# Kernel tuning notes

Measured on AMD Instinct MI355X. Metric: run time of the kernel, lower is better.

## Reference

```python
import jax, jax.numpy as jnp
import numpy as np

N_NODES = 100000


def _gcn_conv(x, W, b, src, dst, num_nodes):
    """PyG-style GCNConv: add self-loops, symmetric normalization, linear.
    x: [N, Fin], W: [Fin, Fout], b: [Fout], src/dst: [E] (already include self-loops).
    """
    h = x @ W  # [N, Fout] transform first (PyG order), keeps edge traffic at Fout width
    ones = jnp.ones(dst.shape[0], dtype=h.dtype)
    deg = jax.ops.segment_sum(ones, dst, num_segments=num_nodes)  # degree of A+I
    dinv = jnp.where(deg > 0, jax.lax.rsqrt(deg), 0.0)
    norm = dinv[src] * dinv[dst]  # [E]
    msg = h[src] * norm[:, None]  # [E, Fout] gather + scale
    out = jax.ops.segment_sum(msg, dst, num_segments=num_nodes)  # scatter-add
    return out + b


def setup_inputs() -> dict:
    key = jax.random.key(0)
    k1, k2, k3, k4, k5 = jax.random.split(key, 5)
    input_dim, hidden_dim, embedding_dim = 128, 64, 32
    x = jax.random.normal(k1, (N_NODES, input_dim), dtype=jnp.float32)
    edge_index = jax.random.randint(k2, (2, 1600000), 0, N_NODES, dtype=jnp.int32)
    # Glorot-like init for weights
    W1 = jax.random.normal(k3, (input_dim, hidden_dim), dtype=jnp.float32) / np.sqrt(input_dim)
    b1 = jnp.zeros((hidden_dim,), dtype=jnp.float32)
    W2 = jax.random.normal(k4, (hidden_dim, embedding_dim), dtype=jnp.float32) / np.sqrt(hidden_dim)
    b2 = jnp.zeros((embedding_dim,), dtype=jnp.float32)
    return {"x": x, "edge_index": edge_index, "W1": W1, "b1": b1, "W2": W2, "b2": b2}


def reference(x, edge_index, W1, b1, W2, b2):
    num_nodes = x.shape[0]
    loop = jnp.arange(num_nodes, dtype=edge_index.dtype)
    src = jnp.concatenate([edge_index[0], loop])  # add self-loops (PyG default)
    dst = jnp.concatenate([edge_index[1], loop])
    h = _gcn_conv(x, W1, b1, src, dst, num_nodes)
    h = jax.nn.relu(h)
    z = _gcn_conv(h, W2, b2, src, dst, num_nodes)
    return z
```

## Files before the change

### kernel.cpp

```cpp
#include <hip/hip_runtime.h>
#include <hip/hip_bf16.h>


#define MAXBUCK 512

typedef unsigned int uint32;

__device__ __forceinline__ void fma4(float4& a, float s, const float4& w) {
    a.x = fmaf(s, w.x, a.x); a.y = fmaf(s, w.y, a.y);
    a.z = fmaf(s, w.z, a.z); a.w = fmaf(s, w.w, a.w);
}
__device__ __forceinline__ uint32 bf16rn(float f) {
    uint32 u = __float_as_uint(f);
    return (u + 0x7fffu + ((u >> 16) & 1u)) >> 16;
}
__device__ __forceinline__ float bflo(uint32 v) { return __uint_as_float(v << 16); }
__device__ __forceinline__ float bfhi(uint32 v) { return __uint_as_float(v & 0xffff0000u); }

__global__ void k_initcur(int* __restrict__ cursor, int nbuck, int cap) {
    int i = blockIdx.x * blockDim.x + threadIdx.x;
    if (i < nbuck) cursor[i] = i * cap;
}

__global__ __launch_bounds__(1024) void k_bin(const int* __restrict__ src,
                                              const int* __restrict__ dst, int E,
                                              int nbuck, int cap,
                                              int* __restrict__ cursor,
                                              uint32* __restrict__ pairs) {
    __shared__ int hist[MAXBUCK];
    __shared__ int base_l[MAXBUCK];
    __shared__ int cur[MAXBUCK];
    int t = threadIdx.x;
    int e0 = blockIdx.x * 4096;
    for (int i = t; i < MAXBUCK; i += 1024) { hist[i] = 0; cur[i] = 0; }
    __syncthreads();
    for (int i = t; i < 4096; i += 1024) {
        int e = e0 + i;
        if (e < E) atomicAdd(&hist[dst[e] >> 8], 1);
    }
    __syncthreads();
    for (int i = t; i < nbuck; i += 1024)
        base_l[i] = hist[i] ? atomicAdd(&cursor[i], hist[i]) : 0;
    __syncthreads();
    for (int i = t; i < 4096; i += 1024) {
        int e = e0 + i;
        if (e < E) {
            int d = dst[e];
            int b = d >> 8;
            int p = atomicAdd(&cur[b], 1);
            int idx = base_l[b] + p;
            if (idx < (b + 1) * cap)
                pairs[idx] = (uint32)src[e] | ((uint32)(d & 255) << 24);
        }
    }
}

__global__ __launch_bounds__(1024) void k_fill2(const uint32* __restrict__ pairs,
                                                const int* __restrict__ bucket_end,
                                                int cap, int N,
                                                int* __restrict__ srclist,
                                                int* __restrict__ rowstart,
                                                int* __restrict__ cnt,
                                                float* __restrict__ dinv) {
    __shared__ int hist[256];
    __shared__ int sh[256];
    __shared__ int rs_ex[256];
    __shared__ int cur[256];
    int b = blockIdx.x;
    int t = threadIdx.x;
    int start = b * cap;
    int end = min(bucket_end[b], start + cap);
    int node0 = b << 8;

    if (t < 256) { hist[t] = 0; cur[t] = 0; }
    __syncthreads();
    for (int e = start + t; e < end; e += 1024)
        atomicAdd(&hist[pairs[e] >> 24], 1);
    __syncthreads();
    int v = 0;
    if (t < 256) { v = hist[t]; sh[t] = v; }
    __syncthreads();
    for (int off = 1; off < 256; off <<= 1) {
        int tmp = 0;
        if (t < 256 && t >= off) tmp = sh[t - off];
        __syncthreads();
        if (t < 256) sh[t] += tmp;
        __syncthreads();
    }
    if (t < 256) {
        rs_ex[t] = sh[t] - v;
        int node = node0 + t;
        if (node < N) {
            rowstart[node] = start + rs_ex[t];
            cnt[node] = v;
            dinv[node] = rsqrtf((float)(v + 1));
        }
    }
    __syncthreads();
    for (int e = start + t; e < end; e += 1024) {
        uint32 pr = pairs[e];
        int dl = pr >> 24;
        int p = atomicAdd(&cur[dl], 1);
        srclist[start + rs_ex[dl] + p] = (int)(pr & 0x00FFFFFFu);
    }
}

__global__ __launch_bounds__(256) void k_gemm1(const float* __restrict__ x,
                                               const float* __restrict__ W1,
                                               const float* __restrict__ dinv,
                                               uint32* __restrict__ h1b, int n) {
    __shared__ float W1s[128 * 64];
    __shared__ float xs[32][132];
    int t = threadIdx.x;
    const float4* W1v = (const float4*)W1;
    float4* W1sv = (float4*)W1s;
    for (int i = t; i < 2048; i += 256) W1sv[i] = W1v[i];
    int node0 = blockIdx.x * 32;
    const float4* xv = (const float4*)x;
    for (int i = t; i < 1024; i += 256) {
        int nl = i >> 5, kq = i & 31;
        int node = node0 + nl;
        float4 v = make_float4(0.f, 0.f, 0.f, 0.f);
        if (node < n) v = xv[(size_t)node * 32 + kq];
        *(float4*)&xs[nl][kq * 4] = v;
    }
    __syncthreads();

    int tx = t & 15;
    int ty = t >> 4;
    int na = ty * 2, nb = na + 1;
    float4 acc0 = make_float4(0.f, 0.f, 0.f, 0.f);
    float4 acc1 = make_float4(0.f, 0.f, 0.f, 0.f);
    const float4* W1sq = (const float4*)W1s;
#pragma unroll 4
    for (int kq = 0; kq < 32; kq++) {
        float4 xa = *(const float4*)&xs[na][kq * 4];
        float4 xb = *(const float4*)&xs[nb][kq * 4];
        float4 w0 = W1sq[(kq * 4 + 0) * 16 + tx];
        float4 w1 = W1sq[(kq * 4 + 1) * 16 + tx];
        float4 w2 = W1sq[(kq * 4 + 2) * 16 + tx];
        float4 w3 = W1sq[(kq * 4 + 3) * 16 + tx];
        fma4(acc0, xa.x, w0); fma4(acc0, xa.y, w1);
        fma4(acc0, xa.z, w2); fma4(acc0, xa.w, w3);
        fma4(acc1, xb.x, w0); fma4(acc1, xb.y, w1);
        fma4(acc1, xb.z, w2); fma4(acc1, xb.w, w3);
    }
    int nA = node0 + na, nB = node0 + nb;
    if (nA < n) {
        float di = dinv[nA];
        uint2 pk = make_uint2(bf16rn(acc0.x * di) | (bf16rn(acc0.y * di) << 16),
                              bf16rn(acc0.z * di) | (bf16rn(acc0.w * di) << 16));
        ((uint2*)h1b)[(size_t)nA * 16 + tx] = pk;
    }
    if (nB < n) {
        float di = dinv[nB];
        uint2 pk = make_uint2(bf16rn(acc1.x * di) | (bf16rn(acc1.y * di) << 16),
                              bf16rn(acc1.z * di) | (bf16rn(acc1.w * di) << 16));
        ((uint2*)h1b)[(size_t)nB * 16 + tx] = pk;
    }
}

__global__ __launch_bounds__(256) void k_gather_l1(const int* __restrict__ rowstart,
                                                   const int* __restrict__ cnt,
                                                   const int* __restrict__ srclist,
                                                   const uint32* __restrict__ h1b,
                                                   const float* __restrict__ dinv,
                                                   const float* __restrict__ b1,
                                                   const float* __restrict__ W2,
                                                   unsigned short* __restrict__ h2b, int n) {
    __shared__ __align__(16) float W2s[64 * 32];
    __shared__ __align__(16) float hb[4][64];
    int t = threadIdx.x;
    {
        const float4* W2v = (const float4*)W2;
        float4* W2sv = (float4*)W2s;
        W2sv[t] = W2v[t];
        W2sv[t + 256] = W2v[t + 256];
    }
    int wid = t >> 6, lane = t & 63;
    int node = blockIdx.x * 4 + wid;
    bool valid = (node < n);
    int j = lane & 15, q = lane >> 4;

    int row = valid ? rowstart[node] : 0;
    int m_all = valid ? cnt[node] : 0;
    float di = valid ? dinv[node] : 0.0f;
    const uint2* h1v = (const uint2*)h1b;
    float a0 = 0.f, a1 = 0.f, a2 = 0.f, a3 = 0.f;
    for (int j0 = 0; j0 < m_all; j0 += 64) {
        int m = min(64, m_all - j0);
        int sidx = (lane < m) ? srclist[row + j0 + lane] : 0;
        int jj = 0;
        for (; jj + 16 <= m; jj += 16) {
            int s0 = __shfl(sidx, jj + q);
            int s1 = __shfl(sidx, jj + 4 + q);
            int s2 = __shfl(sidx, jj + 8 + q);
            int s3 = __shfl(sidx, jj + 12 + q);
            uint2 v0 = h1v[(size_t)s0 * 16 + j];
            uint2 v1 = h1v[(size_t)s1 * 16 + j];
            uint2 v2 = h1v[(size_t)s2 * 16 + j];
            uint2 v3 = h1v[(size_t)s3 * 16 + j];
            a0 += (bflo(v0.x) + bflo(v1.x)) + (bflo(v2.x) + bflo(v3.x));
            a1 += (bfhi(v0.x) + bfhi(v1.x)) + (bfhi(v2.x) + bfhi(v3.x));
            a2 += (bflo(v0.y) + bflo(v1.y)) + (bflo(v2.y) + bflo(v3.y));
            a3 += (bfhi(v0.y) + bfhi(v1.y)) + (bfhi(v2.y) + bfhi(v3.y));
        }
        for (; jj + 8 <= m; jj += 8) {
            int s0 = __shfl(sidx, jj + q);
            int s1 = __shfl(sidx, jj + 4 + q);
            uint2 v0 = h1v[(size_t)s0 * 16 + j];
            uint2 v1 = h1v[(size_t)s1 * 16 + j];
            a0 += bflo(v0.x) + bflo(v1.x);
            a1 += bfhi(v0.x) + bfhi(v1.x);
            a2 += bflo(v0.y) + bflo(v1.y);
            a3 += bfhi(v0.y) + bfhi(v1.y);
        }
        for (; jj < m; jj += 4) {
            int jidx = jj + q;
            int s = __shfl(sidx, min(jidx, m - 1));
            uint2 v = h1v[(size_t)s * 16 + j];
            if (jidx < m) {
                a0 += bflo(v.x); a1 += bfhi(v.x);
                a2 += bflo(v.y); a3 += bfhi(v.y);
            }
        }
    }
    a0 += __shfl_xor(a0, 16); a0 += __shfl_xor(a0, 32);
    a1 += __shfl_xor(a1, 16); a1 += __shfl_xor(a1, 32);
    a2 += __shfl_xor(a2, 16); a2 += __shfl_xor(a2, 32);
    a3 += __shfl_xor(a3, 16); a3 += __shfl_xor(a3, 32);
    if (valid && q == 0) {
        uint2 sv = h1v[(size_t)node * 16 + j];
        float4 bq = ((const float4*)b1)[j];
        float4 hv;
        hv.x = fmaxf((a0 + bflo(sv.x)) * di + bq.x, 0.0f);
        hv.y = fmaxf((a1 + bfhi(sv.x)) * di + bq.y, 0.0f);
        hv.z = fmaxf((a2 + bflo(sv.y)) * di + bq.z, 0.0f);
        hv.w = fmaxf((a3 + bfhi(sv.y)) * di + bq.w, 0.0f);
        *(float4*)&hb[wid][4 * j] = hv;
    }
    __syncthreads();
    if (valid) {
        int c = lane & 31, half = lane >> 5;
        int k0 = half * 32;
        float s = 0.0f;
        const float4* hb4 = (const float4*)&hb[wid][k0];
#pragma unroll
        for (int kk = 0; kk < 8; kk++) {
            float4 h4 = hb4[kk];
            int kb = k0 + kk * 4;
            s = fmaf(h4.x, W2s[(kb + 0) * 32 + c], s);
            s = fmaf(h4.y, W2s[(kb + 1) * 32 + c], s);
            s = fmaf(h4.z, W2s[(kb + 2) * 32 + c], s);
            s = fmaf(h4.w, W2s[(kb + 3) * 32 + c], s);
        }
        s += __shfl_xor(s, 32);
        if (half == 0) h2b[(size_t)node * 32 + c] = (unsigned short)bf16rn(s * di);
    }
}

__global__ __launch_bounds__(256) void k_gather_l2(const int* __restrict__ rowstart,
                                                   const int* __restrict__ cnt,
                                                   const int* __restrict__ srclist,
                                                   const uint32* __restrict__ h2b,
                                                   const float* __restrict__ dinv,
                                                   const float* __restrict__ b2v,
                                                   float* __restrict__ out, int n) {
    int t = threadIdx.x;
    int wid = t >> 6, lane = t & 63;
    int node = blockIdx.x * 4 + wid;
    if (node >= n) return;
    int j = lane & 7, o = lane >> 3;

    int row = rowstart[node], m_all = cnt[node];
    float di = dinv[node];
    const uint2* h2v = (const uint2*)h2b;
    float a0 = 0.f, a1 = 0.f, a2 = 0.f, a3 = 0.f;
    for (int j0 = 0; j0 < m_all; j0 += 64) {
        int m = min(64, m_all - j0);
        int sidx = (lane < m) ? srclist[row + j0 + lane] : 0;
        int jj = 0;
        for (; jj + 16 <= m; jj += 16) {
            int s0 = __shfl(sidx, jj + o);
            int s1 = __shfl(sidx, jj + 8 + o);
            uint2 v0 = h2v[(size_t)s0 * 8 + j];
            uint2 v1 = h2v[(size_t)s1 * 8 + j];
            a0 += bflo(v0.x) + bflo(v1.x);
            a1 += bfhi(v0.x) + bfhi(v1.x);
            a2 += bflo(v0.y) + bflo(v1.y);
            a3 += bfhi(v0.y) + bfhi(v1.y);
        }
        for (; jj + 8 <= m; jj += 8) {
            int s0 = __shfl(sidx, jj + o);
            uint2 v0 = h2v[(size_t)s0 * 8 + j];
            a0 += bflo(v0.x); a1 += bfhi(v0.x);
            a2 += bflo(v0.y); a3 += bfhi(v0.y);
        }
        if (jj < m) {
            int jidx = jj + o;
            int s = __shfl(sidx, min(jidx, m - 1));
            uint2 v = h2v[(size_t)s * 8 + j];
            if (jidx < m) {
                a0 += bflo(v.x); a1 += bfhi(v.x);
                a2 += bflo(v.y); a3 += bfhi(v.y);
            }
        }
    }
    a0 += __shfl_xor(a0, 8); a0 += __shfl_xor(a0, 16); a0 += __shfl_xor(a0, 32);
    a1 += __shfl_xor(a1, 8); a1 += __shfl_xor(a1, 16); a1 += __shfl_xor(a1, 32);
    a2 += __shfl_xor(a2, 8); a2 += __shfl_xor(a2, 16); a2 += __shfl_xor(a2, 32);
    a3 += __shfl_xor(a3, 8); a3 += __shfl_xor(a3, 16); a3 += __shfl_xor(a3, 32);
    if (o == 0) {
        float di2 = di;
        uint2 sv = h2v[(size_t)node * 8 + j];
        float4 bq = ((const float4*)b2v)[j];
        float4 ov;
        ov.x = (a0 + bflo(sv.x)) * di2 + bq.x;
        ov.y = (a1 + bfhi(sv.x)) * di2 + bq.y;
        ov.z = (a2 + bflo(sv.y)) * di2 + bq.z;
        ov.w = (a3 + bfhi(sv.y)) * di2 + bq.w;
        ((float4*)out)[(size_t)node * 8 + j] = ov;
    }
}

extern "C" void kernel_launch(void* const* d_in, const int* in_sizes, int n_in,
                              void* d_out, int out_size, void* d_ws, size_t ws_size,
                              hipStream_t stream) {
    const float* x  = (const float*)d_in[0];
    const int*   ei = (const int*)d_in[1];
    const float* W1 = (const float*)d_in[2];
    const float* b1 = (const float*)d_in[3];
    const float* W2 = (const float*)d_in[4];
    const float* b2 = (const float*)d_in[5];
    float* out = (float*)d_out;

    const int N = in_sizes[0] / 128;
    const int E = in_sizes[1] / 2;
    const int* src = ei;
    const int* dst = ei + E;
    const int nbuck = (N + 255) >> 8;

    int mean = (E + nbuck - 1) / nbuck;
    int cap = (mean + (mean >> 3) + 256 + 63) & ~63;
    size_t region = (size_t)nbuck * cap;

    char* p = (char*)d_ws;
    uint32* pairs      = (uint32*)p;    p += region * 4;
    int* srclist       = (int*)p;       p += region * 4;
    uint32* h1b        = (uint32*)p;    p += (size_t)N * 64 * 2;
    uint32* h2b        = (uint32*)p;    p += (size_t)N * 32 * 2;
    int* cursor        = (int*)p;       p += MAXBUCK * 4;
    int* rowstart      = (int*)p;       p += (size_t)N * 4;
    int* cnt           = (int*)p;       p += (size_t)N * 4;
    float* dinv        = (float*)p;     p += (size_t)N * 4;

    k_initcur<<<(nbuck + 255) / 256, 256, 0, stream>>>(cursor, nbuck, cap);
    k_bin<<<(E + 4095) / 4096, 1024, 0, stream>>>(src, dst, E, nbuck, cap, cursor, pairs);
    k_fill2<<<nbuck, 1024, 0, stream>>>(pairs, cursor, cap, N, srclist, rowstart, cnt, dinv);

    k_gemm1<<<(N + 31) / 32, 256, 0, stream>>>(x, W1, dinv, h1b, N);
    k_gather_l1<<<(N + 3) / 4, 256, 0, stream>>>(rowstart, cnt, srclist, h1b, dinv,
                                                 b1, W2, (unsigned short*)h2b, N);
    k_gather_l2<<<(N + 3) / 4, 256, 0, stream>>>(rowstart, cnt, srclist, h2b, dinv,
                                                 b2, out, N);
}
```

Measured before the change: 252.0 us.

## Gather four nodes per wavefront, pack node metadata, pad bucket cursors, split GEMM staging

```diff
diff --git a/kernel.cpp b/kernel.cpp
--- a/kernel.cpp
+++ b/kernel.cpp
@@ -3,6 +3,7 @@
 
 
 #define MAXBUCK 512
+#define CURSTRIDE 16
 
 typedef unsigned int uint32;
 
@@ -16,11 +17,6 @@
 }
 __device__ __forceinline__ float bflo(uint32 v) { return __uint_as_float(v << 16); }
 __device__ __forceinline__ float bfhi(uint32 v) { return __uint_as_float(v & 0xffff0000u); }
-
-__global__ void k_initcur(int* __restrict__ cursor, int nbuck, int cap) {
-    int i = blockIdx.x * blockDim.x + threadIdx.x;
-    if (i < nbuck) cursor[i] = i * cap;
-}
 
 __global__ __launch_bounds__(1024) void k_bin(const int* __restrict__ src,
                                               const int* __restrict__ dst, int E,
@@ -30,22 +26,27 @@
     __shared__ int hist[MAXBUCK];
     __shared__ int base_l[MAXBUCK];
     __shared__ int cur[MAXBUCK];
+    __shared__ int dloc[4096];
     int t = threadIdx.x;
     int e0 = blockIdx.x * 4096;
     for (int i = t; i < MAXBUCK; i += 1024) { hist[i] = 0; cur[i] = 0; }
-    __syncthreads();
-    for (int i = t; i < 4096; i += 1024) {
-        int e = e0 + i;
-        if (e < E) atomicAdd(&hist[dst[e] >> 8], 1);
-    }
-    __syncthreads();
-    for (int i = t; i < nbuck; i += 1024)
-        base_l[i] = hist[i] ? atomicAdd(&cursor[i], hist[i]) : 0;
     __syncthreads();
     for (int i = t; i < 4096; i += 1024) {
         int e = e0 + i;
         if (e < E) {
             int d = dst[e];
+            dloc[i] = d;
+            atomicAdd(&hist[d >> 8], 1);
+        }
+    }
+    __syncthreads();
+    for (int i = t; i < nbuck; i += 1024)
+        base_l[i] = hist[i] ? (i * cap + atomicAdd(&cursor[i * CURSTRIDE], hist[i])) : 0;
+    __syncthreads();
+    for (int i = t; i < 4096; i += 1024) {
+        int e = e0 + i;
+        if (e < E) {
+            int d = dloc[i];
             int b = d >> 8;
             int p = atomicAdd(&cur[b], 1);
             int idx = base_l[b] + p;
@@ -56,11 +57,10 @@
 }
 
 __global__ __launch_bounds__(1024) void k_fill2(const uint32* __restrict__ pairs,
-                                                const int* __restrict__ bucket_end,
+                                                const int* __restrict__ bucket_cnt,
                                                 int cap, int N,
                                                 int* __restrict__ srclist,
-                                                int* __restrict__ rowstart,
-                                                int* __restrict__ cnt,
+                                                int4* __restrict__ meta,
                                                 float* __restrict__ dinv) {
     __shared__ int hist[256];
     __shared__ int sh[256];
@@ -69,7 +69,7 @@
     int b = blockIdx.x;
     int t = threadIdx.x;
     int start = b * cap;
-    int end = min(bucket_end[b], start + cap);
+    int end = start + min(bucket_cnt[b * CURSTRIDE], cap);
     int node0 = b << 8;
 
     if (t < 256) { hist[t] = 0; cur[t] = 0; }
@@ -91,9 +91,9 @@
         rs_ex[t] = sh[t] - v;
         int node = node0 + t;
         if (node < N) {
-            rowstart[node] = start + rs_ex[t];
-            cnt[node] = v;
-            dinv[node] = rsqrtf((float)(v + 1));
+            float dv = rsqrtf((float)(v + 1));
+            meta[node] = make_int4(start + rs_ex[t], v, __float_as_int(dv), 0);
+            dinv[node] = dv;
         }
     }
     __syncthreads();
@@ -109,41 +109,45 @@
                                                const float* __restrict__ W1,
                                                const float* __restrict__ dinv,
                                                uint32* __restrict__ h1b, int n) {
-    __shared__ float W1s[128 * 64];
-    __shared__ float xs[32][132];
+    __shared__ float W1s[64 * 64];
+    __shared__ float xs[32][68];
     int t = threadIdx.x;
-    const float4* W1v = (const float4*)W1;
-    float4* W1sv = (float4*)W1s;
-    for (int i = t; i < 2048; i += 256) W1sv[i] = W1v[i];
     int node0 = blockIdx.x * 32;
-    const float4* xv = (const float4*)x;
-    for (int i = t; i < 1024; i += 256) {
-        int nl = i >> 5, kq = i & 31;
-        int node = node0 + nl;
-        float4 v = make_float4(0.f, 0.f, 0.f, 0.f);
-        if (node < n) v = xv[(size_t)node * 32 + kq];
-        *(float4*)&xs[nl][kq * 4] = v;
-    }
-    __syncthreads();
-
     int tx = t & 15;
     int ty = t >> 4;
     int na = ty * 2, nb = na + 1;
     float4 acc0 = make_float4(0.f, 0.f, 0.f, 0.f);
     float4 acc1 = make_float4(0.f, 0.f, 0.f, 0.f);
+    const float4* W1v = (const float4*)W1;
+    const float4* xv = (const float4*)x;
+    float4* W1sv = (float4*)W1s;
     const float4* W1sq = (const float4*)W1s;
+
+#pragma unroll 1
+    for (int ph = 0; ph < 2; ph++) {
+        __syncthreads();
+        for (int i = t; i < 1024; i += 256) W1sv[i] = W1v[ph * 1024 + i];
+        for (int i = t; i < 512; i += 256) {
+            int nl = i >> 4, kq4 = i & 15;
+            int node = node0 + nl;
+            float4 v = make_float4(0.f, 0.f, 0.f, 0.f);
+            if (node < n) v = xv[(size_t)node * 32 + ph * 16 + kq4];
+            *(float4*)&xs[nl][kq4 * 4] = v;
+        }
+        __syncthreads();
 #pragma unroll 4
-    for (int kq = 0; kq < 32; kq++) {
-        float4 xa = *(const float4*)&xs[na][kq * 4];
-        float4 xb = *(const float4*)&xs[nb][kq * 4];
-        float4 w0 = W1sq[(kq * 4 + 0) * 16 + tx];
-        float4 w1 = W1sq[(kq * 4 + 1) * 16 + tx];
-        float4 w2 = W1sq[(kq * 4 + 2) * 16 + tx];
-        float4 w3 = W1sq[(kq * 4 + 3) * 16 + tx];
-        fma4(acc0, xa.x, w0); fma4(acc0, xa.y, w1);
-        fma4(acc0, xa.z, w2); fma4(acc0, xa.w, w3);
-        fma4(acc1, xb.x, w0); fma4(acc1, xb.y, w1);
-        fma4(acc1, xb.z, w2); fma4(acc1, xb.w, w3);
+        for (int kq = 0; kq < 16; kq++) {
+            float4 xa = *(const float4*)&xs[na][kq * 4];
+            float4 xb = *(const float4*)&xs[nb][kq * 4];
+            float4 w0 = W1sq[(kq * 4 + 0) * 16 + tx];
+            float4 w1 = W1sq[(kq * 4 + 1) * 16 + tx];
+            float4 w2 = W1sq[(kq * 4 + 2) * 16 + tx];
+            float4 w3 = W1sq[(kq * 4 + 3) * 16 + tx];
+            fma4(acc0, xa.x, w0); fma4(acc0, xa.y, w1);
+            fma4(acc0, xa.z, w2); fma4(acc0, xa.w, w3);
+            fma4(acc1, xb.x, w0); fma4(acc1, xb.y, w1);
+            fma4(acc1, xb.z, w2); fma4(acc1, xb.w, w3);
+        }
     }
     int nA = node0 + na, nB = node0 + nb;
     if (nA < n) {
@@ -160,16 +164,62 @@
     }
 }
 
-__global__ __launch_bounds__(256) void k_gather_l1(const int* __restrict__ rowstart,
-                                                   const int* __restrict__ cnt,
+__device__ __forceinline__ void drain_l1(int sidx, int jj, int m0,
+                                         const uint2* __restrict__ h1v, int j, int q,
+                                         float& a0, float& a1, float& a2, float& a3) {
+    for (; jj + 8 <= m0; jj += 8) {
+        int s0 = __shfl(sidx, jj + q), s1 = __shfl(sidx, jj + 4 + q);
+        uint2 v0 = h1v[(size_t)s0 * 16 + j], v1 = h1v[(size_t)s1 * 16 + j];
+        a0 += bflo(v0.x) + bflo(v1.x);
+        a1 += bfhi(v0.x) + bfhi(v1.x);
+        a2 += bflo(v0.y) + bflo(v1.y);
+        a3 += bfhi(v0.y) + bfhi(v1.y);
+    }
+    for (; jj < m0; jj += 4) {
+        int jidx = jj + q;
+        int s = __shfl(sidx, min(jidx, m0 - 1));
+        uint2 v = h1v[(size_t)s * 16 + j];
+        if (jidx < m0) {
+            a0 += bflo(v.x); a1 += bfhi(v.x);
+            a2 += bflo(v.y); a3 += bfhi(v.y);
+        }
+    }
+}
+__device__ __forceinline__ void extra_l1(const int* __restrict__ srclist, int row, int m_all,
+                                         int lane, const uint2* __restrict__ h1v, int j, int q,
+                                         float& a0, float& a1, float& a2, float& a3) {
+    for (int j0 = 64; j0 < m_all; j0 += 64) {
+        int m = min(64, m_all - j0);
+        int sb = (lane < m) ? srclist[row + j0 + lane] : 0;
+        int jj = 0;
+        for (; jj + 8 <= m; jj += 8) {
+            int s0 = __shfl(sb, jj + q), s1 = __shfl(sb, jj + 4 + q);
+            uint2 v0 = h1v[(size_t)s0 * 16 + j], v1 = h1v[(size_t)s1 * 16 + j];
+            a0 += bflo(v0.x) + bflo(v1.x);
+            a1 += bfhi(v0.x) + bfhi(v1.x);
+            a2 += bflo(v0.y) + bflo(v1.y);
+            a3 += bfhi(v0.y) + bfhi(v1.y);
+        }
+        for (; jj < m; jj += 4) {
+            int jidx = jj + q;
+            int s = __shfl(sb, min(jidx, m - 1));
+            uint2 v = h1v[(size_t)s * 16 + j];
+            if (jidx < m) {
+                a0 += bflo(v.x); a1 += bfhi(v.x);
+                a2 += bflo(v.y); a3 += bfhi(v.y);
+            }
+        }
+    }
+}
+
+__global__ __launch_bounds__(256) void k_gather_l1(const int4* __restrict__ meta,
                                                    const int* __restrict__ srclist,
                                                    const uint32* __restrict__ h1b,
-                                                   const float* __restrict__ dinv,
                                                    const float* __restrict__ b1,
                                                    const float* __restrict__ W2,
                                                    unsigned short* __restrict__ h2b, int n) {
     __shared__ __align__(16) float W2s[64 * 32];
-    __shared__ __align__(16) float hb[4][64];
+    __shared__ __align__(16) float hb[16][64];
     int t = threadIdx.x;
     {
         const float4* W2v = (const float4*)W2;
@@ -178,73 +228,121 @@
         W2sv[t + 256] = W2v[t + 256];
     }
     int wid = t >> 6, lane = t & 63;
-    int node = blockIdx.x * 4 + wid;
-    bool valid = (node < n);
+    int nA = blockIdx.x * 16 + wid * 4;
+    int nB = nA + 1, nC = nA + 2, nD = nA + 3;
+    bool vA = (nA < n), vB = (nB < n), vC = (nC < n), vD = (nD < n);
     int j = lane & 15, q = lane >> 4;
-
-    int row = valid ? rowstart[node] : 0;
-    int m_all = valid ? cnt[node] : 0;
-    float di = valid ? dinv[node] : 0.0f;
+    float4 bq = ((const float4*)b1)[j];
+
+    int rowA = 0, mA = 0, rowB = 0, mB = 0, rowC = 0, mC = 0, rowD = 0, mD = 0;
+    float diA = 0.f, diB = 0.f, diC = 0.f, diD = 0.f;
+    uint2 svA = make_uint2(0u, 0u), svB = svA, svC = svA, svD = svA;
     const uint2* h1v = (const uint2*)h1b;
-    float a0 = 0.f, a1 = 0.f, a2 = 0.f, a3 = 0.f;
-    for (int j0 = 0; j0 < m_all; j0 += 64) {
-        int m = min(64, m_all - j0);
-        int sidx = (lane < m) ? srclist[row + j0 + lane] : 0;
-        int jj = 0;
-        for (; jj + 16 <= m; jj += 16) {
-            int s0 = __shfl(sidx, jj + q);
-            int s1 = __shfl(sidx, jj + 4 + q);
-            int s2 = __shfl(sidx, jj + 8 + q);
-            int s3 = __shfl(sidx, jj + 12 + q);
-            uint2 v0 = h1v[(size_t)s0 * 16 + j];
-            uint2 v1 = h1v[(size_t)s1 * 16 + j];
-            uint2 v2 = h1v[(size_t)s2 * 16 + j];
-            uint2 v3 = h1v[(size_t)s3 * 16 + j];
-            a0 += (bflo(v0.x) + bflo(v1.x)) + (bflo(v2.x) + bflo(v3.x));
-            a1 += (bfhi(v0.x) + bfhi(v1.x)) + (bfhi(v2.x) + bfhi(v3.x));
-            a2 += (bflo(v0.y) + bflo(v1.y)) + (bflo(v2.y) + bflo(v3.y));
-            a3 += (bfhi(v0.y) + bfhi(v1.y)) + (bfhi(v2.y) + bfhi(v3.y));
-        }
-        for (; jj + 8 <= m; jj += 8) {
-            int s0 = __shfl(sidx, jj + q);
-            int s1 = __shfl(sidx, jj + 4 + q);
-            uint2 v0 = h1v[(size_t)s0 * 16 + j];
-            uint2 v1 = h1v[(size_t)s1 * 16 + j];
-            a0 += bflo(v0.x) + bflo(v1.x);
-            a1 += bfhi(v0.x) + bfhi(v1.x);
-            a2 += bflo(v0.y) + bflo(v1.y);
-            a3 += bfhi(v0.y) + bfhi(v1.y);
-        }
-        for (; jj < m; jj += 4) {
-            int jidx = jj + q;
-            int s = __shfl(sidx, min(jidx, m - 1));
-            uint2 v = h1v[(size_t)s * 16 + j];
-            if (jidx < m) {
-                a0 += bflo(v.x); a1 += bfhi(v.x);
-                a2 += bflo(v.y); a3 += bfhi(v.y);
-            }
-        }
-    }
-    a0 += __shfl_xor(a0, 16); a0 += __shfl_xor(a0, 32);
-    a1 += __shfl_xor(a1, 16); a1 += __shfl_xor(a1, 32);
-    a2 += __shfl_xor(a2, 16); a2 += __shfl_xor(a2, 32);
-    a3 += __shfl_xor(a3, 16); a3 += __shfl_xor(a3, 32);
-    if (valid && q == 0) {
-        uint2 sv = h1v[(size_t)node * 16 + j];
-        float4 bq = ((const float4*)b1)[j];
+    if (vA) { int4 mv = meta[nA]; rowA = mv.x; mA = mv.y; diA = __int_as_float(mv.z);
+              svA = h1v[(size_t)nA * 16 + j]; }
+    if (vB) { int4 mv = meta[nB]; rowB = mv.x; mB = mv.y; diB = __int_as_float(mv.z);
+              svB = h1v[(size_t)nB * 16 + j]; }
+    if (vC) { int4 mv = meta[nC]; rowC = mv.x; mC = mv.y; diC = __int_as_float(mv.z);
+              svC = h1v[(size_t)nC * 16 + j]; }
+    if (vD) { int4 mv = meta[nD]; rowD = mv.x; mD = mv.y; diD = __int_as_float(mv.z);
+              svD = h1v[(size_t)nD * 16 + j]; }
+    int cA = min(64, mA), cB = min(64, mB), cC = min(64, mC), cD = min(64, mD);
+    int sxA = (lane < cA) ? srclist[rowA + lane] : 0;
+    int sxB = (lane < cB) ? srclist[rowB + lane] : 0;
+    int sxC = (lane < cC) ? srclist[rowC + lane] : 0;
+    int sxD = (lane < cD) ? srclist[rowD + lane] : 0;
+
+    float aA0 = 0.f, aA1 = 0.f, aA2 = 0.f, aA3 = 0.f;
+    float aB0 = 0.f, aB1 = 0.f, aB2 = 0.f, aB3 = 0.f;
+    float aC0 = 0.f, aC1 = 0.f, aC2 = 0.f, aC3 = 0.f;
+    float aD0 = 0.f, aD1 = 0.f, aD2 = 0.f, aD3 = 0.f;
+    int jA = 0, jB = 0, jC = 0, jD = 0;
+    for (; jA + 8 <= cA && jB + 8 <= cB && jC + 8 <= cC && jD + 8 <= cD;
+           jA += 8, jB += 8, jC += 8, jD += 8) {
+        int sA0 = __shfl(sxA, jA + q), sA1 = __shfl(sxA, jA + 4 + q);
+        int sB0 = __shfl(sxB, jB + q), sB1 = __shfl(sxB, jB + 4 + q);
+        int sC0 = __shfl(sxC, jC + q), sC1 = __shfl(sxC, jC + 4 + q);
+        int sD0 = __shfl(sxD, jD + q), sD1 = __shfl(sxD, jD + 4 + q);
+        uint2 vA0 = h1v[(size_t)sA0 * 16 + j], vA1 = h1v[(size_t)sA1 * 16 + j];
+        uint2 vB0 = h1v[(size_t)sB0 * 16 + j], vB1 = h1v[(size_t)sB1 * 16 + j];
+        uint2 vC0 = h1v[(size_t)sC0 * 16 + j], vC1 = h1v[(size_t)sC1 * 16 + j];
+        uint2 vD0 = h1v[(size_t)sD0 * 16 + j], vD1 = h1v[(size_t)sD1 * 16 + j];
+        aA0 += bflo(vA0.x) + bflo(vA1.x); aA1 += bfhi(vA0.x) + bfhi(vA1.x);
+        aA2 += bflo(vA0.y) + bflo(vA1.y); aA3 += bfhi(vA0.y) + bfhi(vA1.y);
+        aB0 += bflo(vB0.x) + bflo(vB1.x); aB1 += bfhi(vB0.x) + bfhi(vB1.x);
+        aB2 += bflo(vB0.y) + bflo(vB1.y); aB3 += bfhi(vB0.y) + bfhi(vB1.y);
+        aC0 += bflo(vC0.x) + bflo(vC1.x); aC1 += bfhi(vC0.x) + bfhi(vC1.x);
+        aC2 += bflo(vC0.y) + bflo(vC1.y); aC3 += bfhi(vC0.y) + bfhi(vC1.y);
+        aD0 += bflo(vD0.x) + bflo(vD1.x); aD1 += bfhi(vD0.x) + bfhi(vD1.x);
+        aD2 += bflo(vD0.y) + bflo(vD1.y); aD3 += bfhi(vD0.y) + bfhi(vD1.y);
+    }
+    drain_l1(sxA, jA, cA, h1v, j, q, aA0, aA1, aA2, aA3);
+    drain_l1(sxB, jB, cB, h1v, j, q, aB0, aB1, aB2, aB3);
+    drain_l1(sxC, jC, cC, h1v, j, q, aC0, aC1, aC2, aC3);
+    drain_l1(sxD, jD, cD, h1v, j, q, aD0, aD1, aD2, aD3);
+    extra_l1(srclist, rowA, mA, lane, h1v, j, q, aA0, aA1, aA2, aA3);
+    extra_l1(srclist, rowB, mB, lane, h1v, j, q, aB0, aB1, aB2, aB3);
+    extra_l1(srclist, rowC, mC, lane, h1v, j, q, aC0, aC1, aC2, aC3);
+    extra_l1(srclist, rowD, mD, lane, h1v, j, q, aD0, aD1, aD2, aD3);
+
+    aA0 += __shfl_xor(aA0, 16); aA0 += __shfl_xor(aA0, 32);
+    aA1 += __shfl_xor(aA1, 16); aA1 += __shfl_xor(aA1, 32);
+    aA2 += __shfl_xor(aA2, 16); aA2 += __shfl_xor(aA2, 32);
+    aA3 += __shfl_xor(aA3, 16); aA3 += __shfl_xor(aA3, 32);
+    aB0 += __shfl_xor(aB0, 16); aB0 += __shfl_xor(aB0, 32);
+    aB1 += __shfl_xor(aB1, 16); aB1 += __shfl_xor(aB1, 32);
+    aB2 += __shfl_xor(aB2, 16); aB2 += __shfl_xor(aB2, 32);
+    aB3 += __shfl_xor(aB3, 16); aB3 += __shfl_xor(aB3, 32);
+    aC0 += __shfl_xor(aC0, 16); aC0 += __shfl_xor(aC0, 32);
+    aC1 += __shfl_xor(aC1, 16); aC1 += __shfl_xor(aC1, 32);
+    aC2 += __shfl_xor(aC2, 16); aC2 += __shfl_xor(aC2, 32);
+    aC3 += __shfl_xor(aC3, 16); aC3 += __shfl_xor(aC3, 32);
+    aD0 += __shfl_xor(aD0, 16); aD0 += __shfl_xor(aD0, 32);
+    aD1 += __shfl_xor(aD1, 16); aD1 += __shfl_xor(aD1, 32);
+    aD2 += __shfl_xor(aD2, 16); aD2 += __shfl_xor(aD2, 32);
+    aD3 += __shfl_xor(aD3, 16); aD3 += __shfl_xor(aD3, 32);
+    if (vA && q == 0) {
         float4 hv;
-        hv.x = fmaxf((a0 + bflo(sv.x)) * di + bq.x, 0.0f);
-        hv.y = fmaxf((a1 + bfhi(sv.x)) * di + bq.y, 0.0f);
-        hv.z = fmaxf((a2 + bflo(sv.y)) * di + bq.z, 0.0f);
-        hv.w = fmaxf((a3 + bfhi(sv.y)) * di + bq.w, 0.0f);
-        *(float4*)&hb[wid][4 * j] = hv;
-    }
-    __syncthreads();
-    if (valid) {
-        int c = lane & 31, half = lane >> 5;
-        int k0 = half * 32;
+        hv.x = fmaxf((aA0 + bflo(svA.x)) * diA + bq.x, 0.0f);
+        hv.y = fmaxf((aA1 + bfhi(svA.x)) * diA + bq.y, 0.0f);
+        hv.z = fmaxf((aA2 + bflo(svA.y)) * diA + bq.z, 0.0f);
+        hv.w = fmaxf((aA3 + bfhi(svA.y)) * diA + bq.w, 0.0f);
+        *(float4*)&hb[wid * 4 + 0][4 * j] = hv;
+    }
+    if (vB && q == 0) {
+        float4 hv;
+        hv.x = fmaxf((aB0 + bflo(svB.x)) * diB + bq.x, 0.0f);
+        hv.y = fmaxf((aB1 + bfhi(svB.x)) * diB + bq.y, 0.0f);
+        hv.z = fmaxf((aB2 + bflo(svB.y)) * diB + bq.z, 0.0f);
+        hv.w = fmaxf((aB3 + bfhi(svB.y)) * diB + bq.w, 0.0f);
+        *(float4*)&hb[wid * 4 + 1][4 * j] = hv;
+    }
+    if (vC && q == 0) {
+        float4 hv;
+        hv.x = fmaxf((aC0 + bflo(svC.x)) * diC + bq.x, 0.0f);
+        hv.y = fmaxf((aC1 + bfhi(svC.x)) * diC + bq.y, 0.0f);
+        hv.z = fmaxf((aC2 + bflo(svC.y)) * diC + bq.z, 0.0f);
+        hv.w = fmaxf((aC3 + bfhi(svC.y)) * diC + bq.w, 0.0f);
+        *(float4*)&hb[wid * 4 + 2][4 * j] = hv;
+    }
+    if (vD && q == 0) {
+        float4 hv;
+        hv.x = fmaxf((aD0 + bflo(svD.x)) * diD + bq.x, 0.0f);
+        hv.y = fmaxf((aD1 + bfhi(svD.x)) * diD + bq.y, 0.0f);
+        hv.z = fmaxf((aD2 + bflo(svD.y)) * diD + bq.z, 0.0f);
+        hv.w = fmaxf((aD3 + bfhi(svD.y)) * diD + bq.w, 0.0f);
+        *(float4*)&hb[wid * 4 + 3][4 * j] = hv;
+    }
+    __syncthreads();
+    int c = lane & 31, half = lane >> 5;
+    int k0 = half * 32;
+#pragma unroll
+    for (int nd = 0; nd < 4; nd++) {
+        int node = nA + nd;
+        if (node >= n) break;
+        float di = (nd == 0) ? diA : (nd == 1) ? diB : (nd == 2) ? diC : diD;
         float s = 0.0f;
-        const float4* hb4 = (const float4*)&hb[wid][k0];
+        const float4* hb4 = (const float4*)&hb[wid * 4 + nd][k0];
 #pragma unroll
         for (int kk = 0; kk < 8; kk++) {
             float4 h4 = hb4[kk];
@@ -259,46 +357,41 @@
     }
 }
 
-__global__ __launch_bounds__(256) void k_gather_l2(const int* __restrict__ rowstart,
-                                                   const int* __restrict__ cnt,
-                                                   const int* __restrict__ srclist,
-                                                   const uint32* __restrict__ h2b,
-                                                   const float* __restrict__ dinv,
-                                                   const float* __restrict__ b2v,
-                                                   float* __restrict__ out, int n) {
-    int t = threadIdx.x;
-    int wid = t >> 6, lane = t & 63;
-    int node = blockIdx.x * 4 + wid;
-    if (node >= n) return;
-    int j = lane & 7, o = lane >> 3;
-
-    int row = rowstart[node], m_all = cnt[node];
-    float di = dinv[node];
-    const uint2* h2v = (const uint2*)h2b;
-    float a0 = 0.f, a1 = 0.f, a2 = 0.f, a3 = 0.f;
-    for (int j0 = 0; j0 < m_all; j0 += 64) {
+__device__ __forceinline__ void drain_l2(int sidx, int jj, int m0,
+                                         const uint2* __restrict__ h2v, int j, int o,
+                                         float& a0, float& a1, float& a2, float& a3) {
+    for (; jj + 8 <= m0; jj += 8) {
+        int s0 = __shfl(sidx, jj + o);
+        uint2 v0 = h2v[(size_t)s0 * 8 + j];
+        a0 += bflo(v0.x); a1 += bfhi(v0.x);
+        a2 += bflo(v0.y); a3 += bfhi(v0.y);
+    }
+    if (jj < m0) {
+        int jidx = jj + o;
+        int s = __shfl(sidx, min(jidx, m0 - 1));
+        uint2 v = h2v[(size_t)s * 8 + j];
+        if (jidx < m0) {
+            a0 += bflo(v.x); a1 += bfhi(v.x);
+            a2 += bflo(v.y); a3 += bfhi(v.y);
+        }
+    }
+}
+__device__ __forceinline__ void extra_l2(const int* __restrict__ srclist, int row, int m_all,
+                                         int lane, const uint2* __restrict__ h2v, int j, int o,
+                                         float& a0, float& a1, float& a2, float& a3) {
+    for (int j0 = 64; j0 < m_all; j0 += 64) {
         int m = min(64, m_all - j0);
-        int sidx = (lane < m) ? srclist[row + j0 + lane] : 0;
+        int sb = (lane < m) ? srclist[row + j0 + lane] : 0;
         int jj = 0;
-        for (; jj + 16 <= m; jj += 16) {
-            int s0 = __shfl(sidx, jj + o);
-            int s1 = __shfl(sidx, jj + 8 + o);
-            uint2 v0 = h2v[(size_t)s0 * 8 + j];
-            uint2 v1 = h2v[(size_t)s1 * 8 + j];
-            a0 += bflo(v0.x) + bflo(v1.x);
-            a1 += bfhi(v0.x) + bfhi(v1.x);
-            a2 += bflo(v0.y) + bflo(v1.y);
-            a3 += bfhi(v0.y) + bfhi(v1.y);
-        }
         for (; jj + 8 <= m; jj += 8) {
-            int s0 = __shfl(sidx, jj + o);
+            int s0 = __shfl(sb, jj + o);
             uint2 v0 = h2v[(size_t)s0 * 8 + j];
             a0 += bflo(v0.x); a1 += bfhi(v0.x);
             a2 += bflo(v0.y); a3 += bfhi(v0.y);
         }
         if (jj < m) {
             int jidx = jj + o;
-            int s = __shfl(sidx, min(jidx, m - 1));
+            int s = __shfl(sb, min(jidx, m - 1));
             uint2 v = h2v[(size_t)s * 8 + j];
             if (jidx < m) {
                 a0 += bflo(v.x); a1 += bfhi(v.x);
@@ -306,20 +399,122 @@
             }
         }
     }
-    a0 += __shfl_xor(a0, 8); a0 += __shfl_xor(a0, 16); a0 += __shfl_xor(a0, 32);
-    a1 += __shfl_xor(a1, 8); a1 += __shfl_xor(a1, 16); a1 += __shfl_xor(a1, 32);
-    a2 += __shfl_xor(a2, 8); a2 += __shfl_xor(a2, 16); a2 += __shfl_xor(a2, 32);
-    a3 += __shfl_xor(a3, 8); a3 += __shfl_xor(a3, 16); a3 += __shfl_xor(a3, 32);
+}
+
+__global__ __launch_bounds__(256) void k_gather_l2(const int4* __restrict__ meta,
+                                                   const int* __restrict__ srclist,
+                                                   const uint32* __restrict__ h2b,
+                                                   const float* __restrict__ b2v,
+                                                   float* __restrict__ out, int n) {
+    int t = threadIdx.x;
+    int wid = t >> 6, lane = t & 63;
+    int nA = blockIdx.x * 16 + wid * 4;
+    if (nA >= n) return;
+    int nB = nA + 1, nC = nA + 2, nD = nA + 3;
+    bool vB_ = (nB < n), vC_ = (nC < n), vD_ = (nD < n);
+    int j = lane & 7, o = lane >> 3;
+    float4 bq = ((const float4*)b2v)[j];
+
+    const uint2* h2v = (const uint2*)h2b;
+    int4 mvA = meta[nA];
+    int rowA = mvA.x, mA = mvA.y;
+    float diA = __int_as_float(mvA.z);
+    uint2 svA = h2v[(size_t)nA * 8 + j];
+    int rowB = 0, mB = 0, rowC = 0, mC = 0, rowD = 0, mD = 0;
+    float diB = 0.f, diC = 0.f, diD = 0.f;
+    uint2 svB = make_uint2(0u, 0u), svC = svB, svD = svB;
+    if (vB_) { int4 mv = meta[nB]; rowB = mv.x; mB = mv.y; diB = __int_as_float(mv.z);
+               svB = h2v[(size_t)nB * 8 + j]; }
+    if (vC_) { int4 mv = meta[nC]; rowC = mv.x; mC = mv.y; diC = __int_as_float(mv.z);
+               svC = h2v[(size_t)nC * 8 + j]; }
+    if (vD_) { int4 mv = meta[nD]; rowD = mv.x; mD = mv.y; diD = __int_as_float(mv.z);
+               svD = h2v[(size_t)nD * 8 + j]; }
+    int cA = min(64, mA), cB = min(64, mB), cC = min(64, mC), cD = min(64, mD);
+    int sxA = (lane < cA) ? srclist[rowA + lane] : 0;
+    int sxB = (lane < cB) ? srclist[rowB + lane] : 0;
+    int sxC = (lane < cC) ? srclist[rowC + lane] : 0;
+    int sxD = (lane < cD) ? srclist[rowD + lane] : 0;
+
+    float aA0 = 0.f, aA1 = 0.f, aA2 = 0.f, aA3 = 0.f;
+    float aB0 = 0.f, aB1 = 0.f, aB2 = 0.f, aB3 = 0.f;
+    float aC0 = 0.f, aC1 = 0.f, aC2 = 0.f, aC3 = 0.f;
+    float aD0 = 0.f, aD1 = 0.f, aD2 = 0.f, aD3 = 0.f;
+    int jA = 0, jB = 0, jC = 0, jD = 0;
+    for (; jA + 8 <= cA && jB + 8 <= cB && jC + 8 <= cC && jD + 8 <= cD;
+           jA += 8, jB += 8, jC += 8, jD += 8) {
+        int sA0 = __shfl(sxA, jA + o);
+        int sB0 = __shfl(sxB, jB + o);
+        int sC0 = __shfl(sxC, jC + o);
+        int sD0 = __shfl(sxD, jD + o);
+        uint2 vA0 = h2v[(size_t)sA0 * 8 + j];
+        uint2 vB0 = h2v[(size_t)sB0 * 8 + j];
+        uint2 vC0 = h2v[(size_t)sC0 * 8 + j];
+        uint2 vD0 = h2v[(size_t)sD0 * 8 + j];
+        aA0 += bflo(vA0.x); aA1 += bfhi(vA0.x);
+        aA2 += bflo(vA0.y); aA3 += bfhi(vA0.y);
+        aB0 += bflo(vB0.x); aB1 += bfhi(vB0.x);
+        aB2 += bflo(vB0.y); aB3 += bfhi(vB0.y);
+        aC0 += bflo(vC0.x); aC1 += bfhi(vC0.x);
+        aC2 += bflo(vC0.y); aC3 += bfhi(vC0.y);
+        aD0 += bflo(vD0.x); aD1 += bfhi(vD0.x);
+        aD2 += bflo(vD0.y); aD3 += bfhi(vD0.y);
+    }
+    drain_l2(sxA, jA, cA, h2v, j, o, aA0, aA1, aA2, aA3);
+    drain_l2(sxB, jB, cB, h2v, j, o, aB0, aB1, aB2, aB3);
+    drain_l2(sxC, jC, cC, h2v, j, o, aC0, aC1, aC2, aC3);
+    drain_l2(sxD, jD, cD, h2v, j, o, aD0, aD1, aD2, aD3);
+    extra_l2(srclist, rowA, mA, lane, h2v, j, o, aA0, aA1, aA2, aA3);
+    extra_l2(srclist, rowB, mB, lane, h2v, j, o, aB0, aB1, aB2, aB3);
+    extra_l2(srclist, rowC, mC, lane, h2v, j, o, aC0, aC1, aC2, aC3);
+    extra_l2(srclist, rowD, mD, lane, h2v, j, o, aD0, aD1, aD2, aD3);
+
+    aA0 += __shfl_xor(aA0, 8); aA0 += __shfl_xor(aA0, 16); aA0 += __shfl_xor(aA0, 32);
+    aA1 += __shfl_xor(aA1, 8); aA1 += __shfl_xor(aA1, 16); aA1 += __shfl_xor(aA1, 32);
+    aA2 += __shfl_xor(aA2, 8); aA2 += __shfl_xor(aA2, 16); aA2 += __shfl_xor(aA2, 32);
+    aA3 += __shfl_xor(aA3, 8); aA3 += __shfl_xor(aA3, 16); aA3 += __shfl_xor(aA3, 32);
+    aB0 += __shfl_xor(aB0, 8); aB0 += __shfl_xor(aB0, 16); aB0 += __shfl_xor(aB0, 32);
+    aB1 += __shfl_xor(aB1, 8); aB1 += __shfl_xor(aB1, 16); aB1 += __shfl_xor(aB1, 32);
+    aB2 += __shfl_xor(aB2, 8); aB2 += __shfl_xor(aB2, 16); aB2 += __shfl_xor(aB2, 32);
+    aB3 += __shfl_xor(aB3, 8); aB3 += __shfl_xor(aB3, 16); aB3 += __shfl_xor(aB3, 32);
+    aC0 += __shfl_xor(aC0, 8); aC0 += __shfl_xor(aC0, 16); aC0 += __shfl_xor(aC0, 32);
+    aC1 += __shfl_xor(aC1, 8); aC1 += __shfl_xor(aC1, 16); aC1 += __shfl_xor(aC1, 32);
+    aC2 += __shfl_xor(aC2, 8); aC2 += __shfl_xor(aC2, 16); aC2 += __shfl_xor(aC2, 32);
+    aC3 += __shfl_xor(aC3, 8); aC3 += __shfl_xor(aC3, 16); aC3 += __shfl_xor(aC3, 32);
+    aD0 += __shfl_xor(aD0, 8); aD0 += __shfl_xor(aD0, 16); aD0 += __shfl_xor(aD0, 32);
+    aD1 += __shfl_xor(aD1, 8); aD1 += __shfl_xor(aD1, 16); aD1 += __shfl_xor(aD1, 32);
+    aD2 += __shfl_xor(aD2, 8); aD2 += __shfl_xor(aD2, 16); aD2 += __shfl_xor(aD2, 32);
+    aD3 += __shfl_xor(aD3, 8); aD3 += __shfl_xor(aD3, 16); aD3 += __shfl_xor(aD3, 32);
     if (o == 0) {
-        float di2 = di;
-        uint2 sv = h2v[(size_t)node * 8 + j];
-        float4 bq = ((const float4*)b2v)[j];
         float4 ov;
-        ov.x = (a0 + bflo(sv.x)) * di2 + bq.x;
-        ov.y = (a1 + bfhi(sv.x)) * di2 + bq.y;
-        ov.z = (a2 + bflo(sv.y)) * di2 + bq.z;
-        ov.w = (a3 + bfhi(sv.y)) * di2 + bq.w;
-        ((float4*)out)[(size_t)node * 8 + j] = ov;
+        ov.x = (aA0 + bflo(svA.x)) * diA + bq.x;
+        ov.y = (aA1 + bfhi(svA.x)) * diA + bq.y;
+        ov.z = (aA2 + bflo(svA.y)) * diA + bq.z;
+        ov.w = (aA3 + bfhi(svA.y)) * diA + bq.w;
+        ((float4*)out)[(size_t)nA * 8 + j] = ov;
+        if (vB_) {
+            float4 ob;
+            ob.x = (aB0 + bflo(svB.x)) * diB + bq.x;
+            ob.y = (aB1 + bfhi(svB.x)) * diB + bq.y;
+            ob.z = (aB2 + bflo(svB.y)) * diB + bq.z;
+            ob.w = (aB3 + bfhi(svB.y)) * diB + bq.w;
+            ((float4*)out)[(size_t)nB * 8 + j] = ob;
+        }
+        if (vC_) {
+            float4 oc;
+            oc.x = (aC0 + bflo(svC.x)) * diC + bq.x;
+            oc.y = (aC1 + bfhi(svC.x)) * diC + bq.y;
+            oc.z = (aC2 + bflo(svC.y)) * diC + bq.z;
+            oc.w = (aC3 + bfhi(svC.y)) * diC + bq.w;
+            ((float4*)out)[(size_t)nC * 8 + j] = oc;
+        }
+        if (vD_) {
+            float4 od;
+            od.x = (aD0 + bflo(svD.x)) * diD + bq.x;
+            od.y = (aD1 + bfhi(svD.x)) * diD + bq.y;
+            od.z = (aD2 + bflo(svD.y)) * diD + bq.z;
+            od.w = (aD3 + bfhi(svD.y)) * diD + bq.w;
+            ((float4*)out)[(size_t)nD * 8 + j] = od;
+        }
     }
 }
 
@@ -349,18 +544,16 @@
     int* srclist       = (int*)p;       p += region * 4;
     uint32* h1b        = (uint32*)p;    p += (size_t)N * 64 * 2;
     uint32* h2b        = (uint32*)p;    p += (size_t)N * 32 * 2;
-    int* cursor        = (int*)p;       p += MAXBUCK * 4;
-    int* rowstart      = (int*)p;       p += (size_t)N * 4;
-    int* cnt           = (int*)p;       p += (size_t)N * 4;
+    int* cursor        = (int*)p;       p += MAXBUCK * CURSTRIDE * 4;
+    int4* meta         = (int4*)p;      p += (size_t)N * 16;
     float* dinv        = (float*)p;     p += (size_t)N * 4;
 
-    k_initcur<<<(nbuck + 255) / 256, 256, 0, stream>>>(cursor, nbuck, cap);
+    hipMemsetAsync(cursor, 0, (size_t)nbuck * CURSTRIDE * 4, stream);
     k_bin<<<(E + 4095) / 4096, 1024, 0, stream>>>(src, dst, E, nbuck, cap, cursor, pairs);
-    k_fill2<<<nbuck, 1024, 0, stream>>>(pairs, cursor, cap, N, srclist, rowstart, cnt, dinv);
+    k_fill2<<<nbuck, 1024, 0, stream>>>(pairs, cursor, cap, N, srclist, meta, dinv);
 
     k_gemm1<<<(N + 31) / 32, 256, 0, stream>>>(x, W1, dinv, h1b, N);
-    k_gather_l1<<<(N + 3) / 4, 256, 0, stream>>>(rowstart, cnt, srclist, h1b, dinv,
-                                                 b1, W2, (unsigned short*)h2b, N);
-    k_gather_l2<<<(N + 3) / 4, 256, 0, stream>>>(rowstart, cnt, srclist, h2b, dinv,
-                                                 b2, out, N);
-}
+    k_gather_l1<<<(N + 15) / 16, 256, 0, stream>>>(meta, srclist, h1b,
+                                                   b1, W2, (unsigned short*)h2b, N);
+    k_gather_l2<<<(N + 15) / 16, 256, 0, stream>>>(meta, srclist, h2b, b2, out, N);
+}
```

After: 243.5 us. 3.4% less time.
